# Performance work log

Hardware: AMD Instinct MI355X
Metric: run time of the kernel (lower is better)

Reference implementation:

```python
import jax, jax.numpy as jnp
import numpy as np

B, S, D, DQKV = 4, 2048, 1024, 1024

def setup_inputs() -> dict:
    key = jax.random.key(0)
    kx, kq, kk, kv = jax.random.split(key, 4)
    scale = 1.0 / np.sqrt(D)
    return {
        "x": jax.random.normal(kx, (B, S, D), dtype=jnp.float32),
        "wq": jax.random.normal(kq, (D, DQKV), dtype=jnp.float32) * scale,
        "wk": jax.random.normal(kk, (D, DQKV), dtype=jnp.float32) * scale,
        "wv": jax.random.normal(kv, (D, DQKV), dtype=jnp.float32) * scale,
    }

def reference(x, wq, wk, wv):
    # QKV projections: [B,S,D] @ [D,Dqkv] -> [B,S,Dqkv]
    q = jnp.einsum('bsd,de->bse', x, wq)
    k = jnp.einsum('bsd,de->bse', x, wk)
    v = jnp.einsum('bsd,de->bse', x, wv)
    # scores: [B,S,S], scaled by sqrt(dim_qkv)
    scores = jnp.einsum('bik,bjk->bij', q, k) / jnp.sqrt(jnp.asarray(DQKV, dtype=x.dtype))
    attn = jax.nn.softmax(scores, axis=-1)
    # output: [B,S,Dqkv]
    return jnp.einsum('bij,bjd->bid', attn, v)
```

## Files before the change

### kernel.cpp

```cpp
#include <hip/hip_runtime.h>
#include <cstdint>
#include <cstddef>

typedef __bf16 bf16;
typedef __bf16 bf16x4 __attribute__((ext_vector_type(4)));
typedef __bf16 bf16x8 __attribute__((ext_vector_type(8)));
typedef float  f32x4  __attribute__((ext_vector_type(4)));

#define BATCH 4
#define SEQ   2048
#define DIM   1024
#define LDP   2112

__device__ __forceinline__ bf16 to_bf16(float f) {
    unsigned u = __builtin_bit_cast(unsigned, f);
    u += 0x7fffu + ((u >> 16) & 1u);
    unsigned short h = (unsigned short)(u >> 16);
    return __builtin_bit_cast(bf16, h);
}

__device__ __forceinline__ void load16_lds(const bf16* g, bf16* l) {
    __builtin_amdgcn_global_load_lds(
        (__attribute__((address_space(1))) void*)(g),
        (__attribute__((address_space(3))) void*)(l),
        16, 0, 0);
}

#define BARRIER() do { asm volatile("" ::: "memory"); \
                       __builtin_amdgcn_s_barrier();  \
                       asm volatile("" ::: "memory"); } while (0)
#define LGKM0()   asm volatile("s_waitcnt lgkmcnt(0)" ::: "memory")
#define VM0()     asm volatile("s_waitcnt vmcnt(0)" ::: "memory")
#define VM6()     asm volatile("s_waitcnt vmcnt(6)" ::: "memory")


__device__ __forceinline__ void stage_half(
    const bf16* __restrict__ srcRow0, int ld, int k0, bf16* dstHalfBase)
{
    const int tid  = threadIdx.x;
    const int wave = tid >> 6;
    const int lane = tid & 63;
    const int rg   = lane >> 3;
    const int scoff = ((lane & 7) ^ rg) * 8;
#pragma unroll
    for (int j = 0; j < 2; ++j) {
        const int r = wave * 16 + j * 8;
        load16_lds(srcRow0 + (size_t)(r + rg) * ld + k0 + scoff,
                   dstHalfBase + r * 64);
    }
}

__device__ __forceinline__ void gemm_big_core(
    const bf16* __restrict__ Ablk, const bf16* __restrict__ Bblk,
    int K, int lda, int ldb, bf16* As, bf16* Bs, f32x4 acc[8][4])
{
    const int tid  = threadIdx.x;
    const int lane = tid & 63;
    const int wave = tid >> 6;
    const int wr   = wave >> 2;
    const int wc   = wave & 3;
    const int r16  = lane & 15;
    const int g    = lane >> 4;
    const int r7   = r16 & 7;
    const int pk0  = ((g) ^ r7) * 8;
    const int pk1  = ((4 + g) ^ r7) * 8;
    const int arow = (wr * 128 + r16) * 64;
    const int brow = (wc * 64 + r16) * 64;
    const int NT   = K >> 6;

    stage_half(Bblk, ldb, 0, Bs);
    stage_half(Bblk + (size_t)128 * ldb, ldb, 0, Bs + 8192);
    stage_half(Ablk, lda, 0, As);
    stage_half(Ablk + (size_t)128 * lda, lda, 0, As + 8192);
    VM0();
    BARRIER();

#pragma unroll 2
    for (int t = 0; t < NT; ++t) {
        bf16* Ac = As + (t & 1) * 16384;
        bf16* Bc = Bs + (t & 1) * 16384;
        bf16* An = As + ((t + 1) & 1) * 16384;
        bf16* Bn = Bs + ((t + 1) & 1) * 16384;
        const int k1 = (t + 1) << 6;

        bf16x8 b[4][2], a[4][2], a2[4][2];
#pragma unroll
        for (int n = 0; n < 4; ++n) {
            b[n][0] = *(const bf16x8*)(Bc + brow + n * 1024 + pk0);
            b[n][1] = *(const bf16x8*)(Bc + brow + n * 1024 + pk1);
        }
#pragma unroll
        for (int m = 0; m < 4; ++m) {
            a[m][0] = *(const bf16x8*)(Ac + arow + m * 1024 + pk0);
            a[m][1] = *(const bf16x8*)(Ac + arow + m * 1024 + pk1);
        }
        if (t + 1 < NT) {
            stage_half(Bblk, ldb, k1, Bn);
            stage_half(Bblk + (size_t)128 * ldb, ldb, k1, Bn + 8192);
            stage_half(Ablk, lda, k1, An);
            stage_half(Ablk + (size_t)128 * lda, lda, k1, An + 8192);
        }
#pragma unroll
        for (int m = 0; m < 4; ++m)
#pragma unroll
            for (int n = 0; n < 4; ++n)
#pragma unroll
                for (int ks = 0; ks < 2; ++ks)
                    acc[m][n] = __builtin_amdgcn_mfma_f32_16x16x32_bf16(
                        a[m][ks], b[n][ks], acc[m][n], 0, 0, 0);
#pragma unroll
        for (int m = 0; m < 4; ++m) {
            a2[m][0] = *(const bf16x8*)(Ac + arow + 4096 + m * 1024 + pk0);
            a2[m][1] = *(const bf16x8*)(Ac + arow + 4096 + m * 1024 + pk1);
        }
#pragma unroll
        for (int m = 0; m < 4; ++m)
#pragma unroll
            for (int n = 0; n < 4; ++n)
#pragma unroll
                for (int ks = 0; ks < 2; ++ks)
                    acc[4 + m][n] = __builtin_amdgcn_mfma_f32_16x16x32_bf16(
                        a2[m][ks], b[n][ks], acc[4 + m][n], 0, 0, 0);

        LGKM0();
        if (t + 1 < NT) VM0();
        BARRIER();
    }
}

__device__ __forceinline__ void gemm_p3_core(
    const bf16* __restrict__ Ablk, const bf16* __restrict__ Bblk,
    int K, int lda, int ldb, bf16* As, bf16* Bs, f32x4 acc[4][4])
{
    const int tid  = threadIdx.x;
    const int lane = tid & 63;
    const int wave = tid >> 6;
    const int wr   = wave >> 1;
    const int wc   = wave & 1;
    const int r16  = lane & 15;
    const int g    = lane >> 4;
    const int r7   = r16 & 7;
    const int pk0  = ((g) ^ r7) * 8;
    const int pk1  = ((4 + g) ^ r7) * 8;
    const int arow = (wr * 64 + r16) * 64;
    const int brow = (wc * 64 + r16) * 64;
    const int NT   = K >> 6;

    stage_half(Ablk, lda, 0, As);
    stage_half(Ablk + (size_t)128 * lda, lda, 0, As + 8192);
    stage_half(Bblk, ldb, 0, Bs);
    stage_half(Ablk, lda, 64, As + 16384);
    stage_half(Ablk + (size_t)128 * lda, lda, 64, As + 16384 + 8192);
    stage_half(Bblk, ldb, 64, Bs + 8192);
    VM6();
    BARRIER();

    int c0 = 0, c2 = 2;
    for (int t = 0; t < NT; ++t) {
        bf16* Ac = As + c0 * 16384;
        bf16* Bc = Bs + c0 * 8192;

        bf16x8 a[4][2], b[4][2];
#pragma unroll
        for (int n = 0; n < 4; ++n) {
            b[n][0] = *(const bf16x8*)(Bc + brow + n * 1024 + pk0);
            b[n][1] = *(const bf16x8*)(Bc + brow + n * 1024 + pk1);
        }
#pragma unroll
        for (int m = 0; m < 4; ++m) {
            a[m][0] = *(const bf16x8*)(Ac + arow + m * 1024 + pk0);
            a[m][1] = *(const bf16x8*)(Ac + arow + m * 1024 + pk1);
        }
        if (t + 2 < NT) {
            const int k2 = (t + 2) << 6;
            bf16* An = As + c2 * 16384;
            bf16* Bn = Bs + c2 * 8192;
            stage_half(Ablk, lda, k2, An);
            stage_half(Ablk + (size_t)128 * lda, lda, k2, An + 8192);
            stage_half(Bblk, ldb, k2, Bn);
        }
#pragma unroll
        for (int m = 0; m < 4; ++m)
#pragma unroll
            for (int n = 0; n < 4; ++n)
#pragma unroll
                for (int ks = 0; ks < 2; ++ks)
                    acc[m][n] = __builtin_amdgcn_mfma_f32_16x16x32_bf16(
                        a[m][ks], b[n][ks], acc[m][n], 0, 0, 0);

        LGKM0();
        if (t + 1 < NT) {
            if (t + 2 < NT) { VM6(); } else { VM0(); }
        }
        BARRIER();
        c0 = (c0 == 2) ? 0 : c0 + 1;
        c2 = (c2 == 2) ? 0 : c2 + 1;
    }
}

__device__ __forceinline__ void write_c256(
    bf16* __restrict__ Cb, int ldc, const f32x4 acc[8][4])
{
    const int lane = threadIdx.x & 63;
    const int wave = threadIdx.x >> 6;
    const int wr = wave >> 2, wc = wave & 3;
    const int r16 = lane & 15, g = lane >> 4;
    const int row0 = wr * 128 + g * 4;
    const int col0 = wc * 64 + r16;
#pragma unroll
    for (int m = 0; m < 8; ++m)
#pragma unroll
        for (int n = 0; n < 4; ++n)
#pragma unroll
            for (int rr = 0; rr < 4; ++rr)
                Cb[(size_t)(row0 + m * 16 + rr) * ldc + col0 + n * 16] =
                    to_bf16(acc[m][n][rr]);
}

__global__ __launch_bounds__(512, 2) void proj_qk(
    const bf16* __restrict__ xb, const bf16* __restrict__ Wt,
    bf16* __restrict__ Q, bf16* __restrict__ Kb)
{
    __shared__ bf16 As[32768];
    __shared__ bf16 Bs[32768];
    f32x4 acc[8][4] = {};

    const int p = blockIdx.x;
    const int x = p & 7, s = p >> 3;
    const int my = x * 4 + (s >> 3);
    const int j  = s & 7;
    const bf16* Ab = xb + (size_t)my * 256 * DIM;
    const bf16* Bb = Wt + (size_t)((j >> 2) ? DIM * DIM : 0)
                        + (size_t)(j & 3) * 256 * DIM;
    bf16* dst = (j >> 2) ? Kb : Q;
    bf16* Cb = dst + (size_t)my * 256 * DIM + (size_t)(j & 3) * 256;

    gemm_big_core(Ab, Bb, DIM, DIM, DIM, As, Bs, acc);
    write_c256(Cb, DIM, acc);
}

__global__ __launch_bounds__(512, 2) void proj_v(
    const bf16* __restrict__ xb, const bf16* __restrict__ Wt,
    bf16* __restrict__ Vt)
{
    __shared__ bf16 As[49152];
    __shared__ bf16 Bs[24576];
    f32x4 acc[4][4] = {};

    const int p = blockIdx.x;
    const int x = p & 7, s = p >> 3;
    const int bz = x & 3;
    const int vx = (x >> 2) * 8 + (s & 7);
    const int vy = s >> 3;
    const bf16* Ab = Wt + (size_t)2 * DIM * DIM + (size_t)vy * 256 * DIM;
    const bf16* Bb = xb + (size_t)bz * SEQ * DIM + (size_t)vx * 128 * DIM;
    bf16* Cb = Vt + (size_t)bz * DIM * LDP + (size_t)vy * 256 * LDP
                  + (size_t)vx * 128;

    gemm_p3_core(Ab, Bb, DIM, DIM, DIM, As, Bs, acc);

    const int lane = threadIdx.x & 63;
    const int wave = threadIdx.x >> 6;
    const int wr = wave >> 1, wc = wave & 1;
    const int r16 = lane & 15, g = lane >> 4;
    const int row0 = wr * 64 + g * 4;
    const int col0 = wc * 64 + r16;
#pragma unroll
    for (int m = 0; m < 4; ++m)
#pragma unroll
        for (int n = 0; n < 4; ++n)
#pragma unroll
            for (int rr = 0; rr < 4; ++rr)
                Cb[(size_t)(row0 + m * 16 + rr) * LDP + col0 + n * 16] =
                    to_bf16(acc[m][n][rr]);
}

__global__ __launch_bounds__(512, 2) void gemm_scores8(
    const bf16* __restrict__ Qm, const bf16* __restrict__ Kb,
    bf16* __restrict__ P, float* __restrict__ lsum)
{
    __shared__ bf16 As[32768];
    __shared__ bf16 Bs[32768];
    f32x4 acc[8][4] = {};

    const int p = blockIdx.x;
    const int x = p & 7, s = p >> 3;
    const int bz = x & 3;
    const int by = (x >> 2) * 4 + (s >> 3);
    const int bx = s & 7;
    const bf16* Ab = Qm + (size_t)bz * SEQ * DIM + (size_t)by * 256 * DIM;
    const bf16* Bb = Kb + (size_t)bz * SEQ * DIM + (size_t)bx * 256 * DIM;
    gemm_big_core(Ab, Bb, DIM, DIM, DIM, As, Bs, acc);

    bf16* Cb  = P + (size_t)bz * SEQ * LDP;
    float* ls = lsum + (size_t)bz * SEQ;
    const int lane = threadIdx.x & 63;
    const int wave = threadIdx.x >> 6;
    const int wr = wave >> 2, wc = wave & 3;
    const int r16 = lane & 15, g = lane >> 4;
    const int rowB = by * 256 + wr * 128 + g * 4;
    const int colB = bx * 256 + wc * 64 + r16;
#pragma unroll
    for (int m = 0; m < 8; ++m)
#pragma unroll
        for (int rr = 0; rr < 4; ++rr) {
            float sum = 0.0f;
#pragma unroll
            for (int n = 0; n < 4; ++n) {
                const float e = __expf(acc[m][n][rr] * 0.03125f);
                sum += e;
                Cb[(size_t)(rowB + m * 16 + rr) * LDP + colB + n * 16] = to_bf16(e);
            }
            sum += __shfl_xor(sum, 1);
            sum += __shfl_xor(sum, 2);
            sum += __shfl_xor(sum, 4);
            sum += __shfl_xor(sum, 8);
            if (r16 == 0)
                atomicAdd(ls + rowB + m * 16 + rr, sum);
        }
}

__global__ __launch_bounds__(512, 2) void gemm_pv_p3(
    const bf16* __restrict__ P, const bf16* __restrict__ Vt,
    float* __restrict__ C, const float* __restrict__ lsum)
{
    __shared__ bf16 As[49152];
    __shared__ bf16 Bs[24576];
    f32x4 acc[4][4] = {};

    const int p = blockIdx.x;
    const int x = p & 7, s = p >> 3;
    const int bz = x & 3;
    const int by = (x >> 2) * 4 + (s >> 3);
    const int bx = s & 7;
    const bf16* Ab = P  + (size_t)bz * SEQ * LDP + (size_t)by * 256 * LDP;
    const bf16* Bb = Vt + (size_t)bz * DIM * LDP + (size_t)bx * 128 * LDP;
    gemm_p3_core(Ab, Bb, SEQ, LDP, LDP, As, Bs, acc);

    float* Cb = C + (size_t)bz * SEQ * DIM;
    const float* ls = lsum + (size_t)bz * SEQ;
    const int lane = threadIdx.x & 63;
    const int wave = threadIdx.x >> 6;
    const int wr = wave >> 1, wc = wave & 1;
    const int r16 = lane & 15, g = lane >> 4;
    const int row0 = by * 256 + wr * 64 + g * 4;
    const int col0 = bx * 128 + wc * 64 + r16;
#pragma unroll
    for (int m = 0; m < 4; ++m)
#pragma unroll
        for (int rr = 0; rr < 4; ++rr) {
            const int row = row0 + m * 16 + rr;
            const float inv = __builtin_amdgcn_rcpf(ls[row]);
#pragma unroll
            for (int n = 0; n < 4; ++n)
                Cb[(size_t)row * DIM + col0 + n * 16] = acc[m][n][rr] * inv;
        }
}

__global__ __launch_bounds__(256) void prep(
    const float* __restrict__ x,  const float* __restrict__ wq,
    const float* __restrict__ wk, const float* __restrict__ wv,
    bf16* __restrict__ xb, bf16* __restrict__ Wt, float* __restrict__ lsum)
{
    __shared__ float tile[32][33];
    const int b = blockIdx.x;
    const int tid = threadIdx.x;
    if (b < 8192) {
        const size_t i = ((size_t)b * 256 + tid) * 4;
        const float4 v = *(const float4*)(x + i);
        bf16x4 o = { to_bf16(v.x), to_bf16(v.y), to_bf16(v.z), to_bf16(v.w) };
        *(bf16x4*)(xb + i) = o;
    } else if (b < 8192 + 3072) {
        const int t   = b - 8192;
        const int sel = t >> 10;
        const int n0  = (t & 31) * 32;
        const int k0  = ((t >> 5) & 31) * 32;
        const float* w = (sel == 0) ? wq : (sel == 1) ? wk : wv;
        const int tx = tid & 31, ty = tid >> 5;
#pragma unroll
        for (int j = 0; j < 32; j += 8)
            tile[ty + j][tx] = w[(size_t)(k0 + ty + j) * 1024 + n0 + tx];
        __syncthreads();
        bf16* dst = Wt + (size_t)sel * 1024 * 1024;
#pragma unroll
        for (int j = 0; j < 32; j += 8)
            dst[(size_t)(n0 + ty + j) * 1024 + k0 + tx] = to_bf16(tile[tx][ty + j]);
    } else {
#pragma unroll
        for (int i = 0; i < 32; ++i)
            lsum[i * 256 + tid] = 0.0f;
    }
}

extern "C" void kernel_launch(void* const* d_in, const int* in_sizes, int n_in,
                              void* d_out, int out_size, void* d_ws, size_t ws_size,
                              hipStream_t stream)
{
    const float* x  = (const float*)d_in[0];
    const float* wq = (const float*)d_in[1];
    const float* wk = (const float*)d_in[2];
    const float* wv = (const float*)d_in[3];
    float* out = (float*)d_out;
    char* ws = (char*)d_ws;

    bf16*  xb   = (bf16*)(ws);
    bf16*  Wt   = (bf16*)(ws + (16u << 20));
    bf16*  Q    = (bf16*)(ws + (22u << 20));
    bf16*  Kb   = (bf16*)(ws + (38u << 20));
    bf16*  Vt   = (bf16*)(ws + (54u << 20));
    bf16*  P    = (bf16*)(ws + (72u << 20));
    float* lsum = (float*)(ws + (108u << 20));

    prep<<<dim3(8192 + 3072 + 1), dim3(256), 0, stream>>>(
        x, wq, wk, wv, xb, Wt, lsum);

    proj_qk<<<dim3(256), dim3(512), 0, stream>>>(xb, Wt, Q, Kb);
    proj_v<<<dim3(256), dim3(512), 0, stream>>>(xb, Wt, Vt);

    gemm_scores8<<<dim3(256), dim3(512), 0, stream>>>(Q, Kb, P, lsum);

    gemm_pv_p3<<<dim3(256), dim3(512), 0, stream>>>(P, Vt, out, lsum);
}
```

Baseline: 222.9 us.

## Switch QK projection and score GEMMs to 256x128 triple-buffered p3 core

Replaces the 256x256 double-buffered GEMM core used by the Q/K projection and score kernels with the existing 256x128 three-stage pipelined core already used for V and PV. Grids double from 256 to 512 blocks, giving more blocks to spread across compute units and deeper load/compute overlap. In exchange, each block reuses less data per tile, so global traffic per FLOP rises and there are more lsum atomics in the score epilogue.

```diff
diff --git a/kernel.cpp b/kernel.cpp
--- a/kernel.cpp
+++ b/kernel.cpp
@@ -47,84 +47,6 @@
         const int r = wave * 16 + j * 8;
         load16_lds(srcRow0 + (size_t)(r + rg) * ld + k0 + scoff,
                    dstHalfBase + r * 64);
-    }
-}
-
-__device__ __forceinline__ void gemm_big_core(
-    const bf16* __restrict__ Ablk, const bf16* __restrict__ Bblk,
-    int K, int lda, int ldb, bf16* As, bf16* Bs, f32x4 acc[8][4])
-{
-    const int tid  = threadIdx.x;
-    const int lane = tid & 63;
-    const int wave = tid >> 6;
-    const int wr   = wave >> 2;
-    const int wc   = wave & 3;
-    const int r16  = lane & 15;
-    const int g    = lane >> 4;
-    const int r7   = r16 & 7;
-    const int pk0  = ((g) ^ r7) * 8;
-    const int pk1  = ((4 + g) ^ r7) * 8;
-    const int arow = (wr * 128 + r16) * 64;
-    const int brow = (wc * 64 + r16) * 64;
-    const int NT   = K >> 6;
-
-    stage_half(Bblk, ldb, 0, Bs);
-    stage_half(Bblk + (size_t)128 * ldb, ldb, 0, Bs + 8192);
-    stage_half(Ablk, lda, 0, As);
-    stage_half(Ablk + (size_t)128 * lda, lda, 0, As + 8192);
-    VM0();
-    BARRIER();
-
-#pragma unroll 2
-    for (int t = 0; t < NT; ++t) {
-        bf16* Ac = As + (t & 1) * 16384;
-        bf16* Bc = Bs + (t & 1) * 16384;
-        bf16* An = As + ((t + 1) & 1) * 16384;
-        bf16* Bn = Bs + ((t + 1) & 1) * 16384;
-        const int k1 = (t + 1) << 6;
-
-        bf16x8 b[4][2], a[4][2], a2[4][2];
-#pragma unroll
-        for (int n = 0; n < 4; ++n) {
-            b[n][0] = *(const bf16x8*)(Bc + brow + n * 1024 + pk0);
-            b[n][1] = *(const bf16x8*)(Bc + brow + n * 1024 + pk1);
-        }
-#pragma unroll
-        for (int m = 0; m < 4; ++m) {
-            a[m][0] = *(const bf16x8*)(Ac + arow + m * 1024 + pk0);
-            a[m][1] = *(const bf16x8*)(Ac + arow + m * 1024 + pk1);
-        }
-        if (t + 1 < NT) {
-            stage_half(Bblk, ldb, k1, Bn);
-            stage_half(Bblk + (size_t)128 * ldb, ldb, k1, Bn + 8192);
-            stage_half(Ablk, lda, k1, An);
-            stage_half(Ablk + (size_t)128 * lda, lda, k1, An + 8192);
-        }
-#pragma unroll
-        for (int m = 0; m < 4; ++m)
-#pragma unroll
-            for (int n = 0; n < 4; ++n)
-#pragma unroll
-                for (int ks = 0; ks < 2; ++ks)
-                    acc[m][n] = __builtin_amdgcn_mfma_f32_16x16x32_bf16(
-                        a[m][ks], b[n][ks], acc[m][n], 0, 0, 0);
-#pragma unroll
-        for (int m = 0; m < 4; ++m) {
-            a2[m][0] = *(const bf16x8*)(Ac + arow + 4096 + m * 1024 + pk0);
-            a2[m][1] = *(const bf16x8*)(Ac + arow + 4096 + m * 1024 + pk1);
-        }
-#pragma unroll
-        for (int m = 0; m < 4; ++m)
-#pragma unroll
-            for (int n = 0; n < 4; ++n)
-#pragma unroll
-                for (int ks = 0; ks < 2; ++ks)
-                    acc[4 + m][n] = __builtin_amdgcn_mfma_f32_16x16x32_bf16(
-                        a2[m][ks], b[n][ks], acc[4 + m][n], 0, 0, 0);
-
-        LGKM0();
-        if (t + 1 < NT) VM0();
-        BARRIER();
     }
 }
 
@@ -198,17 +120,17 @@
     }
 }
 
-__device__ __forceinline__ void write_c256(
-    bf16* __restrict__ Cb, int ldc, const f32x4 acc[8][4])
+__device__ __forceinline__ void write_c128n(
+    bf16* __restrict__ Cb, int ldc, const f32x4 acc[4][4])
 {
     const int lane = threadIdx.x & 63;
     const int wave = threadIdx.x >> 6;
-    const int wr = wave >> 2, wc = wave & 3;
+    const int wr = wave >> 1, wc = wave & 1;
     const int r16 = lane & 15, g = lane >> 4;
-    const int row0 = wr * 128 + g * 4;
+    const int row0 = wr * 64 + g * 4;
     const int col0 = wc * 64 + r16;
 #pragma unroll
-    for (int m = 0; m < 8; ++m)
+    for (int m = 0; m < 4; ++m)
 #pragma unroll
         for (int n = 0; n < 4; ++n)
 #pragma unroll
@@ -217,26 +139,26 @@
                     to_bf16(acc[m][n][rr]);
 }
 
-__global__ __launch_bounds__(512, 2) void proj_qk(
+__global__ __launch_bounds__(512, 2) void proj_qk_p3(
     const bf16* __restrict__ xb, const bf16* __restrict__ Wt,
     bf16* __restrict__ Q, bf16* __restrict__ Kb)
 {
-    __shared__ bf16 As[32768];
-    __shared__ bf16 Bs[32768];
-    f32x4 acc[8][4] = {};
+    __shared__ bf16 As[49152];
+    __shared__ bf16 Bs[24576];
+    f32x4 acc[4][4] = {};
 
     const int p = blockIdx.x;
     const int x = p & 7, s = p >> 3;
-    const int my = x * 4 + (s >> 3);
-    const int j  = s & 7;
+    const int my = x * 4 + (s >> 4);
+    const int j  = s & 15;
     const bf16* Ab = xb + (size_t)my * 256 * DIM;
-    const bf16* Bb = Wt + (size_t)((j >> 2) ? DIM * DIM : 0)
-                        + (size_t)(j & 3) * 256 * DIM;
-    bf16* dst = (j >> 2) ? Kb : Q;
-    bf16* Cb = dst + (size_t)my * 256 * DIM + (size_t)(j & 3) * 256;
-
-    gemm_big_core(Ab, Bb, DIM, DIM, DIM, As, Bs, acc);
-    write_c256(Cb, DIM, acc);
+    const bf16* Bb = Wt + (size_t)((j >> 3) ? DIM * DIM : 0)
+                        + (size_t)(j & 7) * 128 * DIM;
+    bf16* dst = (j >> 3) ? Kb : Q;
+    bf16* Cb = dst + (size_t)my * 256 * DIM + (size_t)(j & 7) * 128;
+
+    gemm_p3_core(Ab, Bb, DIM, DIM, DIM, As, Bs, acc);
+    write_c128n(Cb, DIM, acc);
 }
 
 __global__ __launch_bounds__(512, 2) void proj_v(
@@ -258,50 +180,36 @@
                   + (size_t)vx * 128;
 
     gemm_p3_core(Ab, Bb, DIM, DIM, DIM, As, Bs, acc);
-
+    write_c128n(Cb, LDP, acc);
+}
+
+__global__ __launch_bounds__(512, 2) void gemm_scores_p3(
+    const bf16* __restrict__ Qm, const bf16* __restrict__ Kb,
+    bf16* __restrict__ P, float* __restrict__ lsum)
+{
+    __shared__ bf16 As[49152];
+    __shared__ bf16 Bs[24576];
+    f32x4 acc[4][4] = {};
+
+    const int p = blockIdx.x;
+    const int x = p & 7, s = p >> 3;
+    const int bz = x & 3;
+    const int by = (x >> 2) * 4 + (s >> 4);
+    const int bx = s & 15;
+    const bf16* Ab = Qm + (size_t)bz * SEQ * DIM + (size_t)by * 256 * DIM;
+    const bf16* Bb = Kb + (size_t)bz * SEQ * DIM + (size_t)bx * 128 * DIM;
+    gemm_p3_core(Ab, Bb, DIM, DIM, DIM, As, Bs, acc);
+
+    bf16* Cb  = P + (size_t)bz * SEQ * LDP;
+    float* ls = lsum + (size_t)bz * SEQ;
     const int lane = threadIdx.x & 63;
     const int wave = threadIdx.x >> 6;
     const int wr = wave >> 1, wc = wave & 1;
     const int r16 = lane & 15, g = lane >> 4;
-    const int row0 = wr * 64 + g * 4;
-    const int col0 = wc * 64 + r16;
+    const int rowB = by * 256 + wr * 64 + g * 4;
+    const int colB = bx * 128 + wc * 64 + r16;
 #pragma unroll
     for (int m = 0; m < 4; ++m)
-#pragma unroll
-        for (int n = 0; n < 4; ++n)
-#pragma unroll
-            for (int rr = 0; rr < 4; ++rr)
-                Cb[(size_t)(row0 + m * 16 + rr) * LDP + col0 + n * 16] =
-                    to_bf16(acc[m][n][rr]);
-}
-
-__global__ __launch_bounds__(512, 2) void gemm_scores8(
-    const bf16* __restrict__ Qm, const bf16* __restrict__ Kb,
-    bf16* __restrict__ P, float* __restrict__ lsum)
-{
-    __shared__ bf16 As[32768];
-    __shared__ bf16 Bs[32768];
-    f32x4 acc[8][4] = {};
-
-    const int p = blockIdx.x;
-    const int x = p & 7, s = p >> 3;
-    const int bz = x & 3;
-    const int by = (x >> 2) * 4 + (s >> 3);
-    const int bx = s & 7;
-    const bf16* Ab = Qm + (size_t)bz * SEQ * DIM + (size_t)by * 256 * DIM;
-    const bf16* Bb = Kb + (size_t)bz * SEQ * DIM + (size_t)bx * 256 * DIM;
-    gemm_big_core(Ab, Bb, DIM, DIM, DIM, As, Bs, acc);
-
-    bf16* Cb  = P + (size_t)bz * SEQ * LDP;
-    float* ls = lsum + (size_t)bz * SEQ;
-    const int lane = threadIdx.x & 63;
-    const int wave = threadIdx.x >> 6;
-    const int wr = wave >> 2, wc = wave & 3;
-    const int r16 = lane & 15, g = lane >> 4;
-    const int rowB = by * 256 + wr * 128 + g * 4;
-    const int colB = bx * 256 + wc * 64 + r16;
-#pragma unroll
-    for (int m = 0; m < 8; ++m)
 #pragma unroll
         for (int rr = 0; rr < 4; ++rr) {
             float sum = 0.0f;
@@ -414,10 +322,10 @@
     prep<<<dim3(8192 + 3072 + 1), dim3(256), 0, stream>>>(
         x, wq, wk, wv, xb, Wt, lsum);
 
-    proj_qk<<<dim3(256), dim3(512), 0, stream>>>(xb, Wt, Q, Kb);
+    proj_qk_p3<<<dim3(512), dim3(512), 0, stream>>>(xb, Wt, Q, Kb);
     proj_v<<<dim3(256), dim3(512), 0, stream>>>(xb, Wt, Vt);
 
-    gemm_scores8<<<dim3(256), dim3(512), 0, stream>>>(Q, Kb, P, lsum);
+    gemm_scores_p3<<<dim3(512), dim3(512), 0, stream>>>(Q, Kb, P, lsum);
 
     gemm_pv_p3<<<dim3(256), dim3(512), 0, stream>>>(P, Vt, out, lsum);
 }
```

Measured after the change: 229.3 us. 2.8% more time.
